# Optimization experiments

Measured on AMD Instinct MI355X. Metric: run time of the kernel, lower is better.

The kernel has to match this reference:

```python
import jax, jax.numpy as jnp
import numpy as np

N, M, D, K = 50000, 32, 128, 8   # nodes, neighbors/node, feature dim, capsules
A = 0.9                          # residual mixing coefficient (self.a)


def setup_inputs() -> dict:
    key = jax.random.key(0)
    k1, k2, k3 = jax.random.split(key, 3)
    x = jax.random.normal(k1, (N, D), dtype=jnp.float32)
    att = jax.random.normal(k2, (2 * D, 1), dtype=jnp.float32) * 0.1
    neighbors = jax.random.randint(k3, (N * M,), 0, N)  # index N would be zero-padding row
    return {"x": x, "att": att, "neighbors": neighbors, "max_iter": 3}


def reference(x, att, neighbors, max_iter):
    n, d = x.shape
    k = K
    dd = d // k                       # delta_d
    m = neighbors.shape[0] // n

    # gather neighbor features (row n is the cached zero pad row)
    z_flat = jnp.concatenate([x, jnp.zeros((1, d), x.dtype)], axis=0)[neighbors]  # (n*m, d)
    z = z_flat.reshape(n, m, k, dd)

    # per-(node, neighbor) scalar attention logit:
    #   e_ij = [x_i ; z_ij.flatten()] @ att,  att: (2d, 1)
    # split the dot product so we never materialize the concatenation
    e_self = x @ att[:d]                                   # (n, 1)
    e_nbr = (z_flat @ att[d:]).reshape(n, m, 1)            # (n, m, 1)
    e = e_self[:, None, :] + e_nbr                          # (n, m, 1)

    # softmax over neighbors (dim=1 in torch); logit is constant over k, so the
    # (n,m,k,1) softmax collapses to (n,m,1)
    attention = jax.nn.softmax(e, axis=1)                   # (n, m, 1)

    # e_prime = sum_dd(attention * z) = attention * sum_dd(z)  -> (n, m, k)
    e_prime = attention * jnp.sum(z, axis=3)

    # NOTE: in the original, the routing variable p is computed each iteration
    # but never used (u never depends on p), so u is identical every iteration
    # and only the FINAL (un-normalized) u is returned:
    #   u = a * sum_m(z * e_prime) + x.view(n, k, dd)
    u = A * jnp.einsum('nmkd,nmk->nkd', z, e_prime) + x.reshape(n, k, dd)
    return u.reshape(n, d)
```

## Files before the change

kernel.cpp:

```cpp
#include <hip/hip_runtime.h>
#include <hip/hip_fp16.h>


#define N_NODES 50000
#define M_NBR   32
#define D_DIM   128
#define A_COEF  0.9f

__global__ __launch_bounds__(256) void to_half_kernel(
    const float4* __restrict__ x4, ushort4* __restrict__ xh4)
{
    const int i = blockIdx.x * 256 + threadIdx.x;
    const float4 v = x4[i];
    ushort4 h;
    h.x = __half_as_ushort(__float2half_rn(v.x));
    h.y = __half_as_ushort(__float2half_rn(v.y));
    h.z = __half_as_ushort(__float2half_rn(v.z));
    h.w = __half_as_ushort(__float2half_rn(v.w));
    xh4[i] = h;
}

__device__ __forceinline__ void unpack8(const uint4& p, float* z) {
    union { unsigned u; __half2 h; } c;
    float2 f;
    c.u = p.x; f = __half22float2(c.h); z[0] = f.x; z[1] = f.y;
    c.u = p.y; f = __half22float2(c.h); z[2] = f.x; z[3] = f.y;
    c.u = p.z; f = __half22float2(c.h); z[4] = f.x; z[5] = f.y;
    c.u = p.w; f = __half22float2(c.h); z[6] = f.x; z[7] = f.y;
}

__global__ __launch_bounds__(256, 4) void routing_main_kernel(
    const float*  __restrict__ x,
    const int*    __restrict__ nbr,
    const __half* __restrict__ xh,
    const float*  __restrict__ att,
    float*        __restrict__ out)
{
    const int lane = threadIdx.x & 63;
    const int g = lane >> 4;
    const int s = lane & 15;
    const int node = __builtin_amdgcn_readfirstlane(
        (int)blockIdx.x * 4 + (int)(threadIdx.x >> 6));

    const float4 a0 = *reinterpret_cast<const float4*>(att + D_DIM + 8 * s);
    const float4 a1 = *reinterpret_cast<const float4*>(att + D_DIM + 8 * s + 4);
    const float4 xs0 = *reinterpret_cast<const float4*>(x + node * D_DIM + 8 * s);
    const float4 xs1 = *reinterpret_cast<const float4*>(x + node * D_DIM + 8 * s + 4);

    const int* nrow = nbr + node * M_NBR;

    uint4 zpk[8];
    float e_[8], t_[8];
    #pragma unroll
    for (int i = 0; i < 8; ++i) {
        int r = nrow[4 * i + g];
        r = min(r, N_NODES - 1);
        zpk[i] = *reinterpret_cast<const uint4*>(xh + (size_t)r * D_DIM + 8 * s);
        float z[8]; unpack8(zpk[i], z);

        const float zs = ((z[0] + z[1]) + (z[2] + z[3]))
                       + ((z[4] + z[5]) + (z[6] + z[7]));
        t_[i] = zs + __shfl_xor(zs, 1);

        float q = z[0] * a0.x + z[1] * a0.y + z[2] * a0.z + z[3] * a0.w
                + z[4] * a1.x + z[5] * a1.y + z[6] * a1.z + z[7] * a1.w;
        q += __shfl_xor(q, 1);
        q += __shfl_xor(q, 2);
        q += __shfl_xor(q, 4);
        q += __shfl_xor(q, 8);
        e_[i] = q;
    }

    float mx = e_[0];
    #pragma unroll
    for (int i = 1; i < 8; ++i) mx = fmaxf(mx, e_[i]);
    mx = fmaxf(mx, __shfl_xor(mx, 16));
    mx = fmaxf(mx, __shfl_xor(mx, 32));

    float p_[8], dsum = 0.f;
    #pragma unroll
    for (int i = 0; i < 8; ++i) { p_[i] = __expf(e_[i] - mx); dsum += p_[i]; }
    dsum += __shfl_xor(dsum, 16);
    dsum += __shfl_xor(dsum, 32);

    float acc[8] = {0.f, 0.f, 0.f, 0.f, 0.f, 0.f, 0.f, 0.f};
    #pragma unroll
    for (int i = 0; i < 8; ++i) {
        float z[8]; unpack8(zpk[i], z);
        const float w = p_[i] * t_[i];
        #pragma unroll
        for (int u = 0; u < 8; ++u) acc[u] = fmaf(z[u], w, acc[u]);
    }

    #pragma unroll
    for (int u = 0; u < 8; ++u) {
        acc[u] += __shfl_xor(acc[u], 16);
        acc[u] += __shfl_xor(acc[u], 32);
    }

    const float scale = A_COEF / dsum;
    if (g == 0) {
        float4 o0, o1;
        o0.x = fmaf(scale, acc[0], xs0.x);
        o0.y = fmaf(scale, acc[1], xs0.y);
        o0.z = fmaf(scale, acc[2], xs0.z);
        o0.w = fmaf(scale, acc[3], xs0.w);
        o1.x = fmaf(scale, acc[4], xs1.x);
        o1.y = fmaf(scale, acc[5], xs1.y);
        o1.z = fmaf(scale, acc[6], xs1.z);
        o1.w = fmaf(scale, acc[7], xs1.w);
        *reinterpret_cast<float4*>(out + node * D_DIM + 8 * s)     = o0;
        *reinterpret_cast<float4*>(out + node * D_DIM + 8 * s + 4) = o1;
    }
}

extern "C" void kernel_launch(void* const* d_in, const int* in_sizes, int n_in,
                              void* d_out, int out_size, void* d_ws, size_t ws_size,
                              hipStream_t stream) {
    const float* x   = (const float*)d_in[0];
    const float* att = (const float*)d_in[1];
    const int*   nbr = (const int*)d_in[2];
    float* out = (float*)d_out;

    __half* xh = (__half*)d_ws;

    to_half_kernel<<<(N_NODES * D_DIM / 4) / 256, 256, 0, stream>>>(
        (const float4*)x, (ushort4*)xh);

    const int grid = N_NODES / 4;
    routing_main_kernel<<<grid, 256, 0, stream>>>(x, nbr, xh, att, out);
}
```

Before: 69.99 us.

## Use packed fp16 dot instructions and transpose-fold shuffle reductions for attention logits

Replaces the per-element half-to-float unpacking and FMA chains for the attention dot product and row sum with v_dot2 fp16 instructions. The 8 separate 16-lane butterfly reductions are replaced by a transpose-style fold that reduces all 8 neighbor logits with fewer shuffles, leaving one logit per lane. Softmax weights are then broadcast with __shfl, and the residual x load moves into the writer lanes only. This cuts ALU and cross-lane traffic, but the attention weights are now rounded to fp16, and the extra broadcast shuffles add some cost back.

Result: faster. 61.94 us (-11.5%).

```diff
diff --git a/kernel.cpp b/kernel.cpp
--- a/kernel.cpp
+++ b/kernel.cpp
@@ -6,6 +6,12 @@
 #define M_NBR   32
 #define D_DIM   128
 #define A_COEF  0.9f
+
+typedef _Float16 h2 __attribute__((ext_vector_type(2)));
+
+__device__ __forceinline__ h2 as_h2(unsigned u) {
+    union { unsigned u; h2 h; } c; c.u = u; return c.h;
+}
 
 __global__ __launch_bounds__(256) void to_half_kernel(
     const float4* __restrict__ x4, ushort4* __restrict__ xh4)
@@ -20,13 +26,16 @@
     xh4[i] = h;
 }
 
-__device__ __forceinline__ void unpack8(const uint4& p, float* z) {
-    union { unsigned u; __half2 h; } c;
-    float2 f;
-    c.u = p.x; f = __half22float2(c.h); z[0] = f.x; z[1] = f.y;
-    c.u = p.y; f = __half22float2(c.h); z[2] = f.x; z[3] = f.y;
-    c.u = p.z; f = __half22float2(c.h); z[4] = f.x; z[5] = f.y;
-    c.u = p.w; f = __half22float2(c.h); z[6] = f.x; z[7] = f.y;
+template<int MASK, int NIN>
+__device__ __forceinline__ void fold_stage(const float* in, float* out, int lane) {
+    const bool hi = (lane & MASK) != 0;
+    #pragma unroll
+    for (int i = 0; i < NIN / 2; ++i) {
+        const float a = in[2 * i], b = in[2 * i + 1];
+        const float send = hi ? a : b;
+        const float recv = __shfl_xor(send, MASK);
+        out[i] = (hi ? b : a) + recv;
+    }
 }
 
 __global__ __launch_bounds__(256, 4) void routing_main_kernel(
@@ -44,52 +53,75 @@
 
     const float4 a0 = *reinterpret_cast<const float4*>(att + D_DIM + 8 * s);
     const float4 a1 = *reinterpret_cast<const float4*>(att + D_DIM + 8 * s + 4);
-    const float4 xs0 = *reinterpret_cast<const float4*>(x + node * D_DIM + 8 * s);
-    const float4 xs1 = *reinterpret_cast<const float4*>(x + node * D_DIM + 8 * s + 4);
+    h2 ah[4];
+    ah[0] = h2{(_Float16)a0.x, (_Float16)a0.y};
+    ah[1] = h2{(_Float16)a0.z, (_Float16)a0.w};
+    ah[2] = h2{(_Float16)a1.x, (_Float16)a1.y};
+    ah[3] = h2{(_Float16)a1.z, (_Float16)a1.w};
+    const h2 ones = h2{(_Float16)1.f, (_Float16)1.f};
 
     const int* nrow = nbr + node * M_NBR;
 
     uint4 zpk[8];
-    float e_[8], t_[8];
     #pragma unroll
     for (int i = 0; i < 8; ++i) {
-        int r = nrow[4 * i + g];
-        r = min(r, N_NODES - 1);
+        const int r = min(nrow[4 * i + g], N_NODES - 1);
         zpk[i] = *reinterpret_cast<const uint4*>(xh + (size_t)r * D_DIM + 8 * s);
-        float z[8]; unpack8(zpk[i], z);
-
-        const float zs = ((z[0] + z[1]) + (z[2] + z[3]))
-                       + ((z[4] + z[5]) + (z[6] + z[7]));
-        t_[i] = zs + __shfl_xor(zs, 1);
-
-        float q = z[0] * a0.x + z[1] * a0.y + z[2] * a0.z + z[3] * a0.w
-                + z[4] * a1.x + z[5] * a1.y + z[6] * a1.z + z[7] * a1.w;
-        q += __shfl_xor(q, 1);
-        q += __shfl_xor(q, 2);
-        q += __shfl_xor(q, 4);
-        q += __shfl_xor(q, 8);
-        e_[i] = q;
     }
 
-    float mx = e_[0];
+    float q[8], t_[8];
     #pragma unroll
-    for (int i = 1; i < 8; ++i) mx = fmaxf(mx, e_[i]);
+    for (int i = 0; i < 8; ++i) {
+        float qq = 0.f, zs = 0.f;
+        qq = __builtin_amdgcn_fdot2(as_h2(zpk[i].x), ah[0], qq, false);
+        qq = __builtin_amdgcn_fdot2(as_h2(zpk[i].y), ah[1], qq, false);
+        qq = __builtin_amdgcn_fdot2(as_h2(zpk[i].z), ah[2], qq, false);
+        qq = __builtin_amdgcn_fdot2(as_h2(zpk[i].w), ah[3], qq, false);
+        zs = __builtin_amdgcn_fdot2(as_h2(zpk[i].x), ones, zs, false);
+        zs = __builtin_amdgcn_fdot2(as_h2(zpk[i].y), ones, zs, false);
+        zs = __builtin_amdgcn_fdot2(as_h2(zpk[i].z), ones, zs, false);
+        zs = __builtin_amdgcn_fdot2(as_h2(zpk[i].w), ones, zs, false);
+        t_[i] = zs + __shfl_xor(zs, 1);
+        q[i] = qq;
+    }
+
+    float f4[4], f2[2], f1[1];
+    fold_stage<1, 8>(q, f4, lane);
+    fold_stage<2, 4>(f4, f2, lane);
+    fold_stage<4, 2>(f2, f1, lane);
+    const float e = f1[0] + __shfl_xor(f1[0], 8);
+
+    float mx = e;
+    mx = fmaxf(mx, __shfl_xor(mx, 1));
+    mx = fmaxf(mx, __shfl_xor(mx, 2));
+    mx = fmaxf(mx, __shfl_xor(mx, 4));
     mx = fmaxf(mx, __shfl_xor(mx, 16));
     mx = fmaxf(mx, __shfl_xor(mx, 32));
+    const float p = __expf(e - mx);
+    float denom = p;
+    denom += __shfl_xor(denom, 1);
+    denom += __shfl_xor(denom, 2);
+    denom += __shfl_xor(denom, 4);
+    denom += __shfl_xor(denom, 16);
+    denom += __shfl_xor(denom, 32);
 
-    float p_[8], dsum = 0.f;
-    #pragma unroll
-    for (int i = 0; i < 8; ++i) { p_[i] = __expf(e_[i] - mx); dsum += p_[i]; }
-    dsum += __shfl_xor(dsum, 16);
-    dsum += __shfl_xor(dsum, 32);
-
+    const int gbase = lane & 0x30;
     float acc[8] = {0.f, 0.f, 0.f, 0.f, 0.f, 0.f, 0.f, 0.f};
     #pragma unroll
     for (int i = 0; i < 8; ++i) {
-        float z[8]; unpack8(zpk[i], z);
-        const float w = p_[i] * t_[i];
-        #pragma unroll
-        for (int u = 0; u < 8; ++u) acc[u] = fmaf(z[u], w, acc[u]);
+        const float wi = __shfl(p, gbase | i) * t_[i];
+        const h2 z01 = as_h2(zpk[i].x);
+        const h2 z23 = as_h2(zpk[i].y);
+        const h2 z45 = as_h2(zpk[i].z);
+        const h2 z67 = as_h2(zpk[i].w);
+        acc[0] = fmaf((float)z01.x, wi, acc[0]);
+        acc[1] = fmaf((float)z01.y, wi, acc[1]);
+        acc[2] = fmaf((float)z23.x, wi, acc[2]);
+        acc[3] = fmaf((float)z23.y, wi, acc[3]);
+        acc[4] = fmaf((float)z45.x, wi, acc[4]);
+        acc[5] = fmaf((float)z45.y, wi, acc[5]);
+        acc[6] = fmaf((float)z67.x, wi, acc[6]);
+        acc[7] = fmaf((float)z67.y, wi, acc[7]);
     }
 
     #pragma unroll
@@ -98,8 +130,10 @@
         acc[u] += __shfl_xor(acc[u], 32);
     }
 
-    const float scale = A_COEF / dsum;
+    const float scale = A_COEF / denom;
     if (g == 0) {
+        const float4 xs0 = *reinterpret_cast<const float4*>(x + node * D_DIM + 8 * s);
+        const float4 xs1 = *reinterpret_cast<const float4*>(x + node * D_DIM + 8 * s + 4);
         float4 o0, o1;
         o0.x = fmaf(scale, acc[0], xs0.x);
         o0.y = fmaf(scale, acc[1], xs0.y);
```
